# Kernel optimization log

Measured on AMD Instinct MI355X. Metric: run time of the kernel, lower is better.

## Reference

```python
import jax, jax.numpy as jnp
import numpy as np

EMBED = 1024
HEADS = 16
HEAD_DIM = EMBED // HEADS


def setup_inputs() -> dict:
    key = jax.random.key(0)
    ks = jax.random.split(key, 9)
    B, S = 1, 4096
    scale = 1.0 / np.sqrt(EMBED)
    x = jax.random.normal(ks[0], (B, S, EMBED), dtype=jnp.float32)
    # nn.Linear weights stored as [out, in]; we store transposed [in, out] for x @ W
    Wq = jax.random.uniform(ks[1], (EMBED, EMBED), jnp.float32, -scale, scale)
    bq = jax.random.uniform(ks[2], (EMBED,), jnp.float32, -scale, scale)
    Wk = jax.random.uniform(ks[3], (EMBED, EMBED), jnp.float32, -scale, scale)
    bk = jax.random.uniform(ks[4], (EMBED,), jnp.float32, -scale, scale)
    Wv = jax.random.uniform(ks[5], (EMBED, EMBED), jnp.float32, -scale, scale)
    bv = jax.random.uniform(ks[6], (EMBED,), jnp.float32, -scale, scale)
    Wo = jax.random.uniform(ks[7], (EMBED, EMBED), jnp.float32, -scale, scale)
    bo = jax.random.uniform(ks[8], (EMBED,), jnp.float32, -scale, scale)
    return {"x": x, "Wq": Wq, "bq": bq, "Wk": Wk, "bk": bk,
            "Wv": Wv, "bv": bv, "Wo": Wo, "bo": bo}


def reference(x, Wq, bq, Wk, bk, Wv, bv, Wo, bo):
    B, S, E = x.shape
    H, D = HEADS, HEAD_DIM
    # projections
    Q = (x @ Wq + bq).reshape(B, S, H, D).transpose(0, 2, 1, 3)  # [B,H,S,D]
    K = (x @ Wk + bk).reshape(B, S, H, D).transpose(0, 2, 1, 3)
    V = (x @ Wv + bv).reshape(B, S, H, D).transpose(0, 2, 1, 3)
    # unfused attention: full [B,H,S,S] score matrix, matching the torch module
    scores = jnp.einsum('bhqd,bhkd->bhqk', Q, K) / jnp.sqrt(jnp.float32(D)).astype(x.dtype)
    probs = jax.nn.softmax(scores, axis=-1)
    out = jnp.einsum('bhqk,bhkd->bhqd', probs, V)  # [B,H,S,D]
    out = out.transpose(0, 2, 1, 3).reshape(B, S, E)
    return out @ Wo + bo
```

## Files before the change

### kernel.cpp

```cpp
#include <hip/hip_runtime.h>


constexpr int Sq = 4096;
constexpr int Ee = 1024;
constexpr int Hh = 16;
constexpr int Dh = 64;

typedef _Float16 half8 __attribute__((ext_vector_type(8)));
typedef _Float16 half4 __attribute__((ext_vector_type(4)));
typedef _Float16 half2t __attribute__((ext_vector_type(2)));
typedef float f32x4 __attribute__((ext_vector_type(4)));

__device__ __forceinline__ unsigned short f2h(float f) {
  _Float16 h = (_Float16)f;
  return *reinterpret_cast<unsigned short*>(&h);
}

__device__ __forceinline__ half2t pk(float a, float b) {
  return __builtin_bit_cast(half2t, __builtin_amdgcn_cvt_pkrtz(a, b));
}

__device__ __forceinline__ void gload16(const void* g, void* l) {
  __builtin_amdgcn_global_load_lds(
      (const __attribute__((address_space(1))) void*)g,
      (__attribute__((address_space(3))) void*)l, 16, 0, 0);
}

__global__ void k_cvt(const float* __restrict__ src, unsigned short* __restrict__ dst) {
  int i = blockIdx.x * blockDim.x + threadIdx.x;
  float4 v = reinterpret_cast<const float4*>(src)[i];
  ushort4 o;
  o.x = f2h(v.x); o.y = f2h(v.y); o.z = f2h(v.z); o.w = f2h(v.w);
  reinterpret_cast<ushort4*>(dst)[i] = o;
}

__global__ void k_twt(const float* __restrict__ W, unsigned short* __restrict__ Wt) {
  __shared__ unsigned short tile[64][65];
  int t = threadIdx.x;
  int kb = blockIdx.x * 64, nb = blockIdx.y * 64;
  int r0 = t >> 4, c4 = (t & 15) * 4;
  for (int i = 0; i < 4; i++) {
    int row = r0 + i * 16;
    float4 v = *reinterpret_cast<const float4*>(W + (size_t)(kb + row) * Ee + nb + c4);
    tile[row][c4 + 0] = f2h(v.x); tile[row][c4 + 1] = f2h(v.y);
    tile[row][c4 + 2] = f2h(v.z); tile[row][c4 + 3] = f2h(v.w);
  }
  __syncthreads();
  for (int i = 0; i < 4; i++) {
    int nrow = r0 + i * 16;
    ushort4 o;
    o.x = tile[c4 + 0][nrow]; o.y = tile[c4 + 1][nrow];
    o.z = tile[c4 + 2][nrow]; o.w = tile[c4 + 3][nrow];
    *reinterpret_cast<ushort4*>(Wt + (size_t)(nb + nrow) * Ee + kb + c4) = o;
  }
}

__global__ void k_tv(const unsigned short* __restrict__ V, unsigned short* __restrict__ Vt) {
  __shared__ unsigned short tile[64][72];
  int t = threadIdx.x;
  int sb = blockIdx.x * 64;
  int h = blockIdx.y;
  const unsigned short* Vh = V + (size_t)h * Sq * Dh;
  unsigned short* Vth = Vt + (size_t)h * Dh * Sq;
  for (int i = 0; i < 2; i++) {
    int c = i * 256 + t;
    int row = c >> 3, dg = c & 7;
    ushort4 a = *reinterpret_cast<const ushort4*>(Vh + (size_t)(sb + row) * Dh + dg * 8);
    ushort4 b = *reinterpret_cast<const ushort4*>(Vh + (size_t)(sb + row) * Dh + dg * 8 + 4);
    *reinterpret_cast<ushort4*>(&tile[row][dg * 8]) = a;
    *reinterpret_cast<ushort4*>(&tile[row][dg * 8 + 4]) = b;
  }
  __syncthreads();
  for (int i = 0; i < 2; i++) {
    int c = i * 256 + t;
    int d = c >> 3, pg = c & 7;
    int p5 = pg >> 2, p4 = (pg >> 1) & 1, p3 = pg & 1;
    int base = p5 * 32 + p4 * 8 + p3 * 4;
    ushort4 o1, o2;
    o1.x = tile[base + 0][d]; o1.y = tile[base + 1][d];
    o1.z = tile[base + 2][d]; o1.w = tile[base + 3][d];
    o2.x = tile[base + 16][d]; o2.y = tile[base + 17][d];
    o2.z = tile[base + 18][d]; o2.w = tile[base + 19][d];
    *reinterpret_cast<ushort4*>(Vth + (size_t)d * Sq + sb + pg * 8) = o1;
    *reinterpret_cast<ushort4*>(Vth + (size_t)d * Sq + sb + pg * 8 + 4) = o2;
  }
}

__global__ __launch_bounds__(256) void k_gemm(
    const unsigned short* __restrict__ A,
    const unsigned short* __restrict__ W0, const unsigned short* __restrict__ W1,
    const unsigned short* __restrict__ W2,
    const float* __restrict__ b0, const float* __restrict__ b1, const float* __restrict__ b2,
    void* d0, void* d1, void* d2, int mode) {
  __shared__ __align__(16) unsigned short Al[128 * 64];
  __shared__ __align__(16) unsigned short Bl[128 * 64];
  const unsigned short* Wt; const float* bias; void* dst;
  if (blockIdx.z == 0)      { Wt = W0; bias = b0; dst = d0; }
  else if (blockIdx.z == 1) { Wt = W1; bias = b1; dst = d1; }
  else                      { Wt = W2; bias = b2; dst = d2; }

  int t = threadIdx.x;
  int w = t >> 6, L = t & 63, quad = L >> 4, c = L & 15;
  int m0 = blockIdx.x * 128, n0 = blockIdx.y * 128;
  int wm = w >> 1, wn = w & 1;

  f32x4 zero = {0.f, 0.f, 0.f, 0.f};
  f32x4 acc[4][4];
#pragma unroll
  for (int i = 0; i < 4; i++)
#pragma unroll
    for (int j = 0; j < 4; j++) acc[i][j] = zero;

  for (int k0 = 0; k0 < 1024; k0 += 64) {
    __syncthreads();
#pragma unroll
    for (int i = 0; i < 4; i++) {
      int ch = i * 256 + t;
      int row = ch >> 3, kgs = ch & 7, kg = kgs ^ (row & 7);
      gload16(A + (size_t)(m0 + row) * 1024 + k0 + kg * 8, &Al[ch * 8]);
    }
#pragma unroll
    for (int i = 0; i < 4; i++) {
      int ch = i * 256 + t;
      int row = ch >> 3, kgs = ch & 7, kg = kgs ^ (row & 7);
      gload16(Wt + (size_t)(n0 + row) * 1024 + k0 + kg * 8, &Bl[ch * 8]);
    }
    __syncthreads();
#pragma unroll
    for (int ks = 0; ks < 2; ks++) {
      half8 af[4], bfr[4];
#pragma unroll
      for (int i = 0; i < 4; i++) {
        int row = wm * 64 + i * 16 + c;
        int kg = (quad + 4 * ks) ^ (row & 7);
        af[i] = *reinterpret_cast<const half8*>(&Al[row * 64 + kg * 8]);
      }
#pragma unroll
      for (int j = 0; j < 4; j++) {
        int row = wn * 64 + j * 16 + c;
        int kg = (quad + 4 * ks) ^ (row & 7);
        bfr[j] = *reinterpret_cast<const half8*>(&Bl[row * 64 + kg * 8]);
      }
#pragma unroll
      for (int i = 0; i < 4; i++)
#pragma unroll
        for (int j = 0; j < 4; j++)
          acc[i][j] = __builtin_amdgcn_mfma_f32_16x16x32_f16(af[i], bfr[j], acc[i][j], 0, 0, 0);
    }
  }

  float sc = (mode == 0 && blockIdx.z == 0) ? 0.18033688011112042f : 1.0f;
#pragma unroll
  for (int j = 0; j < 4; j++) {
    int n = n0 + wn * 64 + j * 16 + c;
    float bv = bias[n];
#pragma unroll
    for (int i = 0; i < 4; i++) {
      int srow = m0 + wm * 64 + i * 16 + quad * 4;
#pragma unroll
      for (int r = 0; r < 4; r++) {
        float v = (acc[i][j][r] + bv) * sc;
        int s = srow + r;
        if (mode == 0) {
          ((unsigned short*)dst)[(size_t)(n >> 6) * Sq * Dh + (size_t)s * Dh + (n & 63)] = f2h(v);
        } else {
          ((float*)dst)[(size_t)s * 1024 + n] = v;
        }
      }
    }
  }
}

__global__ __launch_bounds__(512, 4) void k_attn(
    const unsigned short* __restrict__ Q, const unsigned short* __restrict__ K,
    const unsigned short* __restrict__ Vt, unsigned short* __restrict__ O) {
  __shared__ __align__(16) unsigned short SM[32768];
  int t = threadIdx.x;
  int w = t >> 6, L = t & 63, quad = L >> 4, c = L & 15;
  int wl = w & 3, par = w >> 2;
  int h = blockIdx.y, qb = blockIdx.x;
  const unsigned short* Qh = Q + (size_t)h * Sq * Dh;
  const unsigned short* Kh = K + (size_t)h * Sq * Dh;
  const unsigned short* Vth = Vt + (size_t)h * Dh * Sq;

  half8 qf[2][2];
#pragma unroll
  for (int qg = 0; qg < 2; qg++) {
    int qrow = qb * 128 + wl * 32 + qg * 16 + c;
#pragma unroll
    for (int ks = 0; ks < 2; ks++)
      qf[qg][ks] = *reinterpret_cast<const half8*>(Qh + (size_t)qrow * Dh + ks * 32 + quad * 8);
  }

  f32x4 zero = {0.f, 0.f, 0.f, 0.f};
  f32x4 o0[4], o1[4];
#pragma unroll
  for (int i = 0; i < 4; i++) { o0[i] = zero; o1[i] = zero; }
  f32x4 l0 = zero, l1 = zero;
  half4 ones4;
#pragma unroll
  for (int j = 0; j < 4; j++) ones4[j] = (_Float16)1.0f;

  int srow = t >> 3, skg = (t & 7) ^ (srow & 7);

#pragma unroll
  for (int p2 = 0; p2 < 2; p2++) {
    gload16(Kh + (size_t)(p2 * 64 + srow) * Dh + skg * 8, SM + (0 + p2) * 4096 + t * 8);
    gload16(Vth + (size_t)srow * Sq + p2 * 64 + skg * 8, SM + (2 + p2) * 4096 + t * 8);
  }

  for (int ob = 0; ob < 32; ob++) {
    __syncthreads();
    if (ob < 31) {
      int nb = ob + 1, buf = nb & 1;
#pragma unroll
      for (int p2 = 0; p2 < 2; p2++) {
        int tb = nb * 2 + p2;
        gload16(Kh + (size_t)(tb * 64 + srow) * Dh + skg * 8,
                SM + (buf * 4 + p2) * 4096 + t * 8);
        gload16(Vth + (size_t)srow * Sq + tb * 64 + skg * 8,
                SM + (buf * 4 + 2 + p2) * 4096 + t * 8);
      }
    }
    const unsigned short* Kc = SM + ((ob & 1) * 4 + par) * 4096;
    const unsigned short* Vc = SM + ((ob & 1) * 4 + 2 + par) * 4096;

    f32x4 st0[4], st1[4];
#pragma unroll
    for (int nt = 0; nt < 4; nt++) { st0[nt] = zero; st1[nt] = zero; }
#pragma unroll
    for (int ks = 0; ks < 2; ks++)
#pragma unroll
      for (int nt = 0; nt < 4; nt++) {
        int row = nt * 16 + c;
        half8 kfv = *reinterpret_cast<const half8*>(
            &Kc[row * 64 + (((ks * 4 + quad) ^ (row & 7))) * 8]);
        st0[nt] = __builtin_amdgcn_mfma_f32_16x16x32_f16(kfv, qf[0][ks], st0[nt], 0, 0, 0);
        st1[nt] = __builtin_amdgcn_mfma_f32_16x16x32_f16(kfv, qf[1][ks], st1[nt], 0, 0, 0);
      }

    half4 pb0[4], pb1[4];
#pragma unroll
    for (int nt = 0; nt < 4; nt++) {
      half2t a0 = pk(__builtin_amdgcn_exp2f(st0[nt][0]), __builtin_amdgcn_exp2f(st0[nt][1]));
      half2t a1 = pk(__builtin_amdgcn_exp2f(st0[nt][2]), __builtin_amdgcn_exp2f(st0[nt][3]));
      pb0[nt] = __builtin_shufflevector(a0, a1, 0, 1, 2, 3);
      half2t b0 = pk(__builtin_amdgcn_exp2f(st1[nt][0]), __builtin_amdgcn_exp2f(st1[nt][1]));
      half2t b1 = pk(__builtin_amdgcn_exp2f(st1[nt][2]), __builtin_amdgcn_exp2f(st1[nt][3]));
      pb1[nt] = __builtin_shufflevector(b0, b1, 0, 1, 2, 3);
      l0 = __builtin_amdgcn_mfma_f32_16x16x16f16(ones4, pb0[nt], l0, 0, 0, 0);
      l1 = __builtin_amdgcn_mfma_f32_16x16x16f16(ones4, pb1[nt], l1, 0, 0, 0);
    }

#pragma unroll
    for (int dt = 0; dt < 4; dt++) {
      int row = dt * 16 + c;
#pragma unroll
      for (int n2 = 0; n2 < 2; n2++) {
        half8 vv = *reinterpret_cast<const half8*>(
            &Vc[row * 64 + (((n2 * 4 + quad) ^ (row & 7))) * 8]);
        half4 vlo = __builtin_shufflevector(vv, vv, 0, 1, 2, 3);
        half4 vhi = __builtin_shufflevector(vv, vv, 4, 5, 6, 7);
        o0[dt] = __builtin_amdgcn_mfma_f32_16x16x16f16(vlo, pb0[2 * n2], o0[dt], 0, 0, 0);
        o0[dt] = __builtin_amdgcn_mfma_f32_16x16x16f16(vhi, pb0[2 * n2 + 1], o0[dt], 0, 0, 0);
        o1[dt] = __builtin_amdgcn_mfma_f32_16x16x16f16(vlo, pb1[2 * n2], o1[dt], 0, 0, 0);
        o1[dt] = __builtin_amdgcn_mfma_f32_16x16x16f16(vhi, pb1[2 * n2 + 1], o1[dt], 0, 0, 0);
      }
    }
  }

  __syncthreads();
  float* cb = (float*)SM;
  if (par == 1) {
#pragma unroll
    for (int v = 0; v < 4; v++) {
      *reinterpret_cast<f32x4*>(cb + ((wl * 9 + v) * 64 + L) * 4) = o0[v];
      *reinterpret_cast<f32x4*>(cb + ((wl * 9 + 4 + v) * 64 + L) * 4) = o1[v];
    }
    f32x4 lv = {l0[0], l1[0], 0.f, 0.f};
    *reinterpret_cast<f32x4*>(cb + ((wl * 9 + 8) * 64 + L) * 4) = lv;
  }
  __syncthreads();
  if (par == 0) {
#pragma unroll
    for (int v = 0; v < 4; v++) {
      o0[v] += *reinterpret_cast<const f32x4*>(cb + ((wl * 9 + v) * 64 + L) * 4);
      o1[v] += *reinterpret_cast<const f32x4*>(cb + ((wl * 9 + 4 + v) * 64 + L) * 4);
    }
    f32x4 lv = *reinterpret_cast<const f32x4*>(cb + ((wl * 9 + 8) * 64 + L) * 4);
    float lt0 = l0[0] + lv[0], lt1 = l1[0] + lv[1];

#pragma unroll
    for (int qg = 0; qg < 2; qg++) {
      float inv = 1.f / (qg ? lt1 : lt0);
      f32x4* oo = qg ? o1 : o0;
      int q = qb * 128 + wl * 32 + qg * 16 + c;
#pragma unroll
      for (int dt = 0; dt < 4; dt++) {
        half4 hv;
#pragma unroll
        for (int r = 0; r < 4; r++) hv[r] = (_Float16)(oo[dt][r] * inv);
        *reinterpret_cast<half4*>(&O[(size_t)q * 1024 + h * 64 + dt * 16 + quad * 4]) = hv;
      }
    }
  }
}

extern "C" void kernel_launch(void* const* d_in, const int* in_sizes, int n_in,
                              void* d_out, int out_size, void* d_ws, size_t ws_size,
                              hipStream_t stream) {
  const float* x  = (const float*)d_in[0];
  const float* Wq = (const float*)d_in[1];
  const float* bq = (const float*)d_in[2];
  const float* Wk = (const float*)d_in[3];
  const float* bk = (const float*)d_in[4];
  const float* Wv = (const float*)d_in[5];
  const float* bv = (const float*)d_in[6];
  const float* Wo = (const float*)d_in[7];
  const float* bo = (const float*)d_in[8];

  char* ws = (char*)d_ws;
  const size_t MB = 1u << 20;
  unsigned short* xb  = (unsigned short*)(ws);
  unsigned short* Wqt = (unsigned short*)(ws + 8 * MB);
  unsigned short* Wkt = (unsigned short*)(ws + 10 * MB);
  unsigned short* Wvt = (unsigned short*)(ws + 12 * MB);
  unsigned short* Wot = (unsigned short*)(ws + 14 * MB);
  unsigned short* Qb  = (unsigned short*)(ws + 16 * MB);
  unsigned short* Kb  = (unsigned short*)(ws + 24 * MB);
  unsigned short* Vb  = (unsigned short*)(ws + 32 * MB);
  unsigned short* Vtg = (unsigned short*)(ws + 40 * MB);
  unsigned short* Ob  = (unsigned short*)(ws + 48 * MB);

  k_cvt<<<4096, 256, 0, stream>>>(x, xb);
  dim3 g16(16, 16);
  k_twt<<<g16, 256, 0, stream>>>(Wq, Wqt);
  k_twt<<<g16, 256, 0, stream>>>(Wk, Wkt);
  k_twt<<<g16, 256, 0, stream>>>(Wv, Wvt);
  k_twt<<<g16, 256, 0, stream>>>(Wo, Wot);
  k_gemm<<<dim3(32, 8, 3), 256, 0, stream>>>(xb, Wqt, Wkt, Wvt, bq, bk, bv,
                                             (void*)Qb, (void*)Kb, (void*)Vb, 0);
  k_tv<<<dim3(64, 16), 256, 0, stream>>>(Vb, Vtg);
  k_attn<<<dim3(32, 16), 512, 0, stream>>>(Qb, Kb, Vtg, Ob);
  k_gemm<<<dim3(32, 8, 1), 256, 0, stream>>>(Ob, Wot, Wot, Wot, bo, bo, bo,
                                             d_out, d_out, d_out, 1);
}
```

Measured before the change: 249.4 us.

## Fuse prep kernels, write V transposed from GEMM, use K32 MFMA for PV

Merges the x conversion and the four weight transposes into one launch. The QKV GEMM epilogue now writes V directly in the permuted transposed layout, so the separate V-transpose kernel and its buffer go away. In attention, the probability fragments are packed into half8 and the PV and row-sum products use 16x16x32 MFMA instead of pairs of 16x16x16 ones. This cuts launch count, global traffic and MFMA instruction count, at the cost of strided 8-byte stores in the V epilogue and a dependence on the column permutation matching the K-operand layout.

```diff
diff --git a/kernel.cpp b/kernel.cpp
--- a/kernel.cpp
+++ b/kernel.cpp
@@ -26,18 +26,27 @@
       (__attribute__((address_space(3))) void*)l, 16, 0, 0);
 }
 
-__global__ void k_cvt(const float* __restrict__ src, unsigned short* __restrict__ dst) {
-  int i = blockIdx.x * blockDim.x + threadIdx.x;
-  float4 v = reinterpret_cast<const float4*>(src)[i];
-  ushort4 o;
-  o.x = f2h(v.x); o.y = f2h(v.y); o.z = f2h(v.z); o.w = f2h(v.w);
-  reinterpret_cast<ushort4*>(dst)[i] = o;
-}
-
-__global__ void k_twt(const float* __restrict__ W, unsigned short* __restrict__ Wt) {
+__global__ void k_prep(const float* __restrict__ x,
+                       const float* __restrict__ Wq, const float* __restrict__ Wk,
+                       const float* __restrict__ Wv, const float* __restrict__ Wo,
+                       unsigned short* __restrict__ xb,
+                       unsigned short* __restrict__ Wqt, unsigned short* __restrict__ Wkt,
+                       unsigned short* __restrict__ Wvt, unsigned short* __restrict__ Wot) {
+  int b = blockIdx.x, t = threadIdx.x;
+  if (b < 4096) {
+    int i = b * 256 + t;
+    float4 v = reinterpret_cast<const float4*>(x)[i];
+    ushort4 o;
+    o.x = f2h(v.x); o.y = f2h(v.y); o.z = f2h(v.z); o.w = f2h(v.w);
+    reinterpret_cast<ushort4*>(xb)[i] = o;
+    return;
+  }
   __shared__ unsigned short tile[64][65];
-  int t = threadIdx.x;
-  int kb = blockIdx.x * 64, nb = blockIdx.y * 64;
+  int r = b - 4096;
+  int wi = r >> 8, ti = r & 255;
+  const float* W = (wi == 0) ? Wq : (wi == 1) ? Wk : (wi == 2) ? Wv : Wo;
+  unsigned short* Wt = (wi == 0) ? Wqt : (wi == 1) ? Wkt : (wi == 2) ? Wvt : Wot;
+  int kb = (ti & 15) * 64, nb = (ti >> 4) * 64;
   int r0 = t >> 4, c4 = (t & 15) * 4;
   for (int i = 0; i < 4; i++) {
     int row = r0 + i * 16;
@@ -52,37 +61,6 @@
     o.x = tile[c4 + 0][nrow]; o.y = tile[c4 + 1][nrow];
     o.z = tile[c4 + 2][nrow]; o.w = tile[c4 + 3][nrow];
     *reinterpret_cast<ushort4*>(Wt + (size_t)(nb + nrow) * Ee + kb + c4) = o;
-  }
-}
-
-__global__ void k_tv(const unsigned short* __restrict__ V, unsigned short* __restrict__ Vt) {
-  __shared__ unsigned short tile[64][72];
-  int t = threadIdx.x;
-  int sb = blockIdx.x * 64;
-  int h = blockIdx.y;
-  const unsigned short* Vh = V + (size_t)h * Sq * Dh;
-  unsigned short* Vth = Vt + (size_t)h * Dh * Sq;
-  for (int i = 0; i < 2; i++) {
-    int c = i * 256 + t;
-    int row = c >> 3, dg = c & 7;
-    ushort4 a = *reinterpret_cast<const ushort4*>(Vh + (size_t)(sb + row) * Dh + dg * 8);
-    ushort4 b = *reinterpret_cast<const ushort4*>(Vh + (size_t)(sb + row) * Dh + dg * 8 + 4);
-    *reinterpret_cast<ushort4*>(&tile[row][dg * 8]) = a;
-    *reinterpret_cast<ushort4*>(&tile[row][dg * 8 + 4]) = b;
-  }
-  __syncthreads();
-  for (int i = 0; i < 2; i++) {
-    int c = i * 256 + t;
-    int d = c >> 3, pg = c & 7;
-    int p5 = pg >> 2, p4 = (pg >> 1) & 1, p3 = pg & 1;
-    int base = p5 * 32 + p4 * 8 + p3 * 4;
-    ushort4 o1, o2;
-    o1.x = tile[base + 0][d]; o1.y = tile[base + 1][d];
-    o1.z = tile[base + 2][d]; o1.w = tile[base + 3][d];
-    o2.x = tile[base + 16][d]; o2.y = tile[base + 17][d];
-    o2.z = tile[base + 18][d]; o2.w = tile[base + 19][d];
-    *reinterpret_cast<ushort4*>(Vth + (size_t)d * Sq + sb + pg * 8) = o1;
-    *reinterpret_cast<ushort4*>(Vth + (size_t)d * Sq + sb + pg * 8 + 4) = o2;
   }
 }
 
@@ -149,6 +127,25 @@
     }
   }
 
+  if (mode == 0 && blockIdx.z == 2) {
+    unsigned short* Vt = (unsigned short*)dst;
+#pragma unroll
+    for (int j = 0; j < 4; j++) {
+      int n = n0 + wn * 64 + j * 16 + c;
+      int hh = n >> 6, d = n & 63;
+      float bv = bias[n];
+#pragma unroll
+      for (int i = 0; i < 4; i++) {
+        int pos = m0 + wm * 64 + (i >> 1) * 32 + quad * 8 + (i & 1) * 4;
+        half4 hv;
+#pragma unroll
+        for (int r = 0; r < 4; r++) hv[r] = (_Float16)(acc[i][j][r] + bv);
+        *reinterpret_cast<half4*>(&Vt[(size_t)hh * Dh * Sq + (size_t)d * Sq + pos]) = hv;
+      }
+    }
+    return;
+  }
+
   float sc = (mode == 0 && blockIdx.z == 0) ? 0.18033688011112042f : 1.0f;
 #pragma unroll
   for (int j = 0; j < 4; j++) {
@@ -197,9 +194,9 @@
 #pragma unroll
   for (int i = 0; i < 4; i++) { o0[i] = zero; o1[i] = zero; }
   f32x4 l0 = zero, l1 = zero;
-  half4 ones4;
-#pragma unroll
-  for (int j = 0; j < 4; j++) ones4[j] = (_Float16)1.0f;
+  half8 ones8;
+#pragma unroll
+  for (int j = 0; j < 8; j++) ones8[j] = (_Float16)1.0f;
 
   int srow = t >> 3, skg = (t & 7) ^ (srow & 7);
 
@@ -239,17 +236,25 @@
         st1[nt] = __builtin_amdgcn_mfma_f32_16x16x32_f16(kfv, qf[1][ks], st1[nt], 0, 0, 0);
       }
 
-    half4 pb0[4], pb1[4];
-#pragma unroll
-    for (int nt = 0; nt < 4; nt++) {
-      half2t a0 = pk(__builtin_amdgcn_exp2f(st0[nt][0]), __builtin_amdgcn_exp2f(st0[nt][1]));
-      half2t a1 = pk(__builtin_amdgcn_exp2f(st0[nt][2]), __builtin_amdgcn_exp2f(st0[nt][3]));
-      pb0[nt] = __builtin_shufflevector(a0, a1, 0, 1, 2, 3);
-      half2t b0 = pk(__builtin_amdgcn_exp2f(st1[nt][0]), __builtin_amdgcn_exp2f(st1[nt][1]));
-      half2t b1 = pk(__builtin_amdgcn_exp2f(st1[nt][2]), __builtin_amdgcn_exp2f(st1[nt][3]));
-      pb1[nt] = __builtin_shufflevector(b0, b1, 0, 1, 2, 3);
-      l0 = __builtin_amdgcn_mfma_f32_16x16x16f16(ones4, pb0[nt], l0, 0, 0, 0);
-      l1 = __builtin_amdgcn_mfma_f32_16x16x16f16(ones4, pb1[nt], l1, 0, 0, 0);
+    half8 pB0[2], pB1[2];
+#pragma unroll
+    for (int n2 = 0; n2 < 2; n2++) {
+      half2t a0 = pk(__builtin_amdgcn_exp2f(st0[2 * n2][0]), __builtin_amdgcn_exp2f(st0[2 * n2][1]));
+      half2t a1 = pk(__builtin_amdgcn_exp2f(st0[2 * n2][2]), __builtin_amdgcn_exp2f(st0[2 * n2][3]));
+      half2t a2 = pk(__builtin_amdgcn_exp2f(st0[2 * n2 + 1][0]), __builtin_amdgcn_exp2f(st0[2 * n2 + 1][1]));
+      half2t a3 = pk(__builtin_amdgcn_exp2f(st0[2 * n2 + 1][2]), __builtin_amdgcn_exp2f(st0[2 * n2 + 1][3]));
+      half4 alo = __builtin_shufflevector(a0, a1, 0, 1, 2, 3);
+      half4 ahi = __builtin_shufflevector(a2, a3, 0, 1, 2, 3);
+      pB0[n2] = __builtin_shufflevector(alo, ahi, 0, 1, 2, 3, 4, 5, 6, 7);
+      half2t b0 = pk(__builtin_amdgcn_exp2f(st1[2 * n2][0]), __builtin_amdgcn_exp2f(st1[2 * n2][1]));
+      half2t b1 = pk(__builtin_amdgcn_exp2f(st1[2 * n2][2]), __builtin_amdgcn_exp2f(st1[2 * n2][3]));
+      half2t b2 = pk(__builtin_amdgcn_exp2f(st1[2 * n2 + 1][0]), __builtin_amdgcn_exp2f(st1[2 * n2 + 1][1]));
+      half2t b3 = pk(__builtin_amdgcn_exp2f(st1[2 * n2 + 1][2]), __builtin_amdgcn_exp2f(st1[2 * n2 + 1][3]));
+      half4 blo = __builtin_shufflevector(b0, b1, 0, 1, 2, 3);
+      half4 bhi = __builtin_shufflevector(b2, b3, 0, 1, 2, 3);
+      pB1[n2] = __builtin_shufflevector(blo, bhi, 0, 1, 2, 3, 4, 5, 6, 7);
+      l0 = __builtin_amdgcn_mfma_f32_16x16x32_f16(ones8, pB0[n2], l0, 0, 0, 0);
+      l1 = __builtin_amdgcn_mfma_f32_16x16x32_f16(ones8, pB1[n2], l1, 0, 0, 0);
     }
 
 #pragma unroll
@@ -259,12 +264,8 @@
       for (int n2 = 0; n2 < 2; n2++) {
         half8 vv = *reinterpret_cast<const half8*>(
             &Vc[row * 64 + (((n2 * 4 + quad) ^ (row & 7))) * 8]);
-        half4 vlo = __builtin_shufflevector(vv, vv, 0, 1, 2, 3);
-        half4 vhi = __builtin_shufflevector(vv, vv, 4, 5, 6, 7);
-        o0[dt] = __builtin_amdgcn_mfma_f32_16x16x16f16(vlo, pb0[2 * n2], o0[dt], 0, 0, 0);
-        o0[dt] = __builtin_amdgcn_mfma_f32_16x16x16f16(vhi, pb0[2 * n2 + 1], o0[dt], 0, 0, 0);
-        o1[dt] = __builtin_amdgcn_mfma_f32_16x16x16f16(vlo, pb1[2 * n2], o1[dt], 0, 0, 0);
-        o1[dt] = __builtin_amdgcn_mfma_f32_16x16x16f16(vhi, pb1[2 * n2 + 1], o1[dt], 0, 0, 0);
+        o0[dt] = __builtin_amdgcn_mfma_f32_16x16x32_f16(vv, pB0[n2], o0[dt], 0, 0, 0);
+        o1[dt] = __builtin_amdgcn_mfma_f32_16x16x32_f16(vv, pB1[n2], o1[dt], 0, 0, 0);
       }
     }
   }
@@ -328,19 +329,12 @@
   unsigned short* Wot = (unsigned short*)(ws + 14 * MB);
   unsigned short* Qb  = (unsigned short*)(ws + 16 * MB);
   unsigned short* Kb  = (unsigned short*)(ws + 24 * MB);
-  unsigned short* Vb  = (unsigned short*)(ws + 32 * MB);
-  unsigned short* Vtg = (unsigned short*)(ws + 40 * MB);
-  unsigned short* Ob  = (unsigned short*)(ws + 48 * MB);
-
-  k_cvt<<<4096, 256, 0, stream>>>(x, xb);
-  dim3 g16(16, 16);
-  k_twt<<<g16, 256, 0, stream>>>(Wq, Wqt);
-  k_twt<<<g16, 256, 0, stream>>>(Wk, Wkt);
-  k_twt<<<g16, 256, 0, stream>>>(Wv, Wvt);
-  k_twt<<<g16, 256, 0, stream>>>(Wo, Wot);
+  unsigned short* Vtg = (unsigned short*)(ws + 32 * MB);
+  unsigned short* Ob  = (unsigned short*)(ws + 40 * MB);
+
+  k_prep<<<5120, 256, 0, stream>>>(x, Wq, Wk, Wv, Wo, xb, Wqt, Wkt, Wvt, Wot);
   k_gemm<<<dim3(32, 8, 3), 256, 0, stream>>>(xb, Wqt, Wkt, Wvt, bq, bk, bv,
-                                             (void*)Qb, (void*)Kb, (void*)Vb, 0);
-  k_tv<<<dim3(64, 16), 256, 0, stream>>>(Vb, Vtg);
+                                             (void*)Qb, (void*)Kb, (void*)Vtg, 0);
   k_attn<<<dim3(32, 16), 512, 0, stream>>>(Qb, Kb, Vtg, Ob);
   k_gemm<<<dim3(32, 8, 1), 256, 0, stream>>>(Ob, Wot, Wot, Wot, bo, bo, bo,
                                              d_out, d_out, d_out, 1);
```

New measurement: 236.5 us. 5.1% less time.
